# Optimization experiments

Measured on AMD Instinct MI355X. Metric: run time of the kernel, lower is better.

The kernel has to match this reference:

```python
import jax, jax.numpy as jnp
import numpy as np

NUM_REL = 50000
NUM_EDGES = 1000000
DIM_IN = 128
DIM_OUT = 128
NUM_HEAD = 8
DIM_HID = DIM_OUT // NUM_HEAD


def setup_inputs() -> dict:
    key = jax.random.key(0)
    ks = jax.random.split(key, 5)
    emb_rel = jax.random.normal(ks[0], (NUM_REL, DIM_IN), dtype=jnp.float32)
    relation_triplets = jax.random.randint(ks[1], (NUM_EDGES, 3), 0, NUM_REL, dtype=jnp.int64)
    # xavier-normal-ish scales
    attn_w = jax.random.normal(ks[2], (DIM_OUT, 2 * DIM_IN), dtype=jnp.float32) * np.sqrt(2.0 / (DIM_OUT + 2 * DIM_IN))
    attn_b = jnp.zeros((DIM_OUT,), dtype=jnp.float32)
    attn_vec = jax.random.normal(ks[3], (1, NUM_HEAD, DIM_HID), dtype=jnp.float32) * np.sqrt(2.0 / (NUM_HEAD + DIM_HID))
    aggr_w = jax.random.normal(ks[4], (DIM_OUT, DIM_IN), dtype=jnp.float32) * np.sqrt(2.0 / (DIM_OUT + DIM_IN))
    aggr_b = jnp.zeros((DIM_OUT,), dtype=jnp.float32)
    return {"emb_rel": emb_rel, "relation_triplets": relation_triplets,
            "attn_w": attn_w, "attn_b": attn_b, "attn_vec": attn_vec,
            "aggr_w": aggr_w, "aggr_b": aggr_b}


def reference(emb_rel, relation_triplets, attn_w, attn_b, attn_vec, aggr_w, aggr_b):
    num_rel = emb_rel.shape[0]
    head = relation_triplets[:, 0]
    tail = relation_triplets[:, 1]
    h = emb_rel[head]                         # [E, Din]
    t = emb_rel[tail]                         # [E, Din]
    concat = jnp.concatenate([h, t], axis=-1) # [E, 2*Din]
    # per-edge attention logits
    a = jnp.tanh(concat @ attn_w.T + attn_b).reshape(-1, NUM_HEAD, DIM_HID)
    raw = jnp.sum(a * attn_vec, axis=-1)      # [E, H]
    # segment softmax over edges grouped by head relation
    m = jax.ops.segment_max(raw, head, num_segments=num_rel)   # [R, H]
    ev = jnp.exp(raw - m[head])                                # [E, H]
    s = jax.ops.segment_sum(ev, head, num_segments=num_rel)    # [R, H]
    beta = ev / (s[head] + 1e-16)                              # [E, H]
    # weighted aggregation of projected tail embeddings
    msg = (t @ aggr_w.T + aggr_b).reshape(-1, NUM_HEAD, DIM_HID)  # [E, H, Dh]
    out = jax.ops.segment_sum(beta[..., None] * msg, head, num_segments=num_rel)
    return out.reshape(num_rel, NUM_HEAD * DIM_HID)
```

## Files before the change

kernel.cpp:

```cpp
#include <hip/hip_runtime.h>
#include <hip/hip_bf16.h>

#define DIM 128
#define NHEAD 8
#define CAP_B 64
#define NPART 8
#define CAP8 20
#define MAXD 64

typedef __attribute__((ext_vector_type(8))) short short8;
typedef __attribute__((ext_vector_type(4))) float f32x4;
typedef __attribute__((ext_vector_type(4))) int int4v;

__device__ __forceinline__ unsigned short f2bf(float x) {
    unsigned u = __float_as_uint(x);
    unsigned r = (u + 0x7fffu + ((u >> 16) & 1)) >> 16;
    return (unsigned short)r;
}
__device__ __forceinline__ float bf_lo(unsigned v) { return __uint_as_float(v << 16); }
__device__ __forceinline__ float bf_hi(unsigned v) { return __uint_as_float(v & 0xffff0000u); }

__device__ __forceinline__ float fast_tanh(float x) {
    float e = __expf(2.f * x);
    return 1.f - 2.f * __builtin_amdgcn_rcpf(e + 1.f);
}

__global__ __launch_bounds__(256) void partition_kernel(
    const int4v* __restrict__ trip4, unsigned* __restrict__ binbuf,
    int* __restrict__ blockcnt,
    const float* __restrict__ attn_w, const float* __restrict__ aggr_w,
    unsigned short* __restrict__ w16,
    int nE, int nbP1, int BINS)
{
    if ((int)blockIdx.x >= nbP1) {
        int f = (blockIdx.x - nbP1) * 256 + threadIdx.x;
        if (f >= 3 * 128 * 16) return;
        int m   = f / 2048;
        int rem = f - m * 2048;
        int gc  = rem >> 4;
        int k8  = (rem & 15) * 8;
        const float* src = (m == 2) ? &aggr_w[(size_t)gc * 128 + k8]
                                    : &attn_w[(size_t)gc * 256 + m * 128 + k8];
        float4 v0 = *(const float4*)src;
        float4 v1 = *(const float4*)(src + 4);
        short8 r;
        r[0] = (short)f2bf(v0.x); r[1] = (short)f2bf(v0.y);
        r[2] = (short)f2bf(v0.z); r[3] = (short)f2bf(v0.w);
        r[4] = (short)f2bf(v1.x); r[5] = (short)f2bf(v1.y);
        r[6] = (short)f2bf(v1.z); r[7] = (short)f2bf(v1.w);
        *(short8*)&w16[(size_t)f * 8] = r;
        return;
    }

    __shared__ int hist[64];
    __shared__ int base[64];
    __shared__ int tot;
    __shared__ unsigned recs[1024];
    const int tid = threadIdx.x;
    if (tid < 64) hist[tid] = 0;
    __syncthreads();

    int i = blockIdx.x * 256 + tid;
    int e0 = i * 4;
    int h[4] = {-1, -1, -1, -1}, t[4] = {0, 0, 0, 0};
    if (e0 + 3 < nE) {
        int4v v0 = __builtin_nontemporal_load(&trip4[(size_t)i * 3 + 0]);
        int4v v1 = __builtin_nontemporal_load(&trip4[(size_t)i * 3 + 1]);
        int4v v2 = __builtin_nontemporal_load(&trip4[(size_t)i * 3 + 2]);
        h[0] = v0.x; t[0] = v0.y; h[1] = v0.w; t[1] = v1.x;
        h[2] = v1.z; t[2] = v1.w; h[3] = v2.y; t[3] = v2.z;
    } else if (e0 < nE) {
        const int* trip = (const int*)trip4;
#pragma unroll
        for (int j = 0; j < 4; ++j)
            if (e0 + j < nE) { h[j] = trip[(size_t)(e0 + j) * 3]; t[j] = trip[(size_t)(e0 + j) * 3 + 1]; }
    }

    int bn[4], ofs[4];
#pragma unroll
    for (int j = 0; j < 4; ++j) {
        if (h[j] >= 0) {
            bn[j]  = h[j] >> 10;
            ofs[j] = atomicAdd(&hist[bn[j]], 1);
        }
    }
    __syncthreads();

    if (tid < 64) {
        int v = hist[tid];
        int x = v;
#pragma unroll
        for (int d = 1; d < 64; d <<= 1) {
            int y = __shfl_up(x, d);
            if (tid >= d) x += y;
        }
        base[tid] = x - v;
        if (tid == 63) tot = x;
    }
    __syncthreads();

#pragma unroll
    for (int j = 0; j < 4; ++j)
        if (h[j] >= 0) recs[base[bn[j]] + ofs[j]] = ((unsigned)h[j] << 16) | (unsigned)t[j];
    __syncthreads();

    const int total = tot;
    for (int idx = tid; idx < total; idx += 256) {
        unsigned r = recs[idx];
        int b    = (int)(r >> 26);
        int slot = idx - base[b];
        if (slot < CAP_B)
            binbuf[((size_t)b * nbP1 + blockIdx.x) * CAP_B + slot] = r;
    }
    if (tid < BINS) blockcnt[(size_t)tid * nbP1 + blockIdx.x] = min(hist[tid], CAP_B);
}

__global__ __launch_bounds__(256) void binscatter_kernel(
    const unsigned* __restrict__ binbuf, const int* __restrict__ blockcnt,
    unsigned short* __restrict__ bucket8,
    int* __restrict__ count8,
    int nR, int nbP1)
{
    __shared__ int lcnt[1024];
    __shared__ unsigned short stag[1024 * CAP8];
    __shared__ short bcs[1024];
    const int tid  = threadIdx.x;
    const int b    = blockIdx.x >> 3;
    const int part = blockIdx.x & (NPART - 1);
    const int hbase = b << 10;

    for (int j = tid; j < 1024; j += 256) lcnt[j] = 0;
    for (int j = tid; j < nbP1; j += 256) bcs[j] = (short)blockcnt[(size_t)b * nbP1 + j];
    __syncthreads();

    const int nSeg = (nbP1 > part) ? (nbP1 - part + NPART - 1) / NPART : 0;
    const int totSlots = nSeg * CAP_B;
    for (int f = tid; f < totSlots; f += 256) {
        int k = f >> 6;
        int s = f & 63;
        int j = part + NPART * k;
        if (s < (int)bcs[j]) {
            unsigned r = binbuf[((size_t)b * nbP1 + j) * CAP_B + s];
            int rel  = (int)(r >> 16) - hbase;
            int slot = atomicAdd(&lcnt[rel], 1);
            if (slot < CAP8) stag[rel * CAP8 + slot] = (unsigned short)(r & 0xffffu);
        }
    }
    __syncthreads();

    unsigned* dstw = (unsigned*)(bucket8 + ((size_t)part * nR + hbase) * CAP8);
    const unsigned* srcw = (const unsigned*)stag;
    const int nHead = min(1024, nR - hbase);
    const int nW = nHead * (CAP8 / 2);
    for (int j = tid; j < nW; j += 256) dstw[j] = srcw[j];
    for (int rel = tid; rel < nHead; rel += 256)
        count8[(size_t)part * nR + hbase + rel] = min(lcnt[rel], CAP8);
}

__global__ __launch_bounds__(256) void mfma_precompute_kernel(
    const float* __restrict__ emb,
    const unsigned short* __restrict__ w16,
    const float* __restrict__ attn_b,
    const float* __restrict__ aggr_b,
    unsigned short* __restrict__ hW16,
    unsigned short* __restrict__ twm,
    int R)
{
    const int row0 = blockIdx.x * 64;
    const int wave = threadIdx.x >> 6;
    const int lane = threadIdx.x & 63;
    const int lrow = lane & 15;
    const int kg   = lane >> 4;
    const int kbase = kg * 8;

    short8 a[4][4];
#pragma unroll
    for (int rt = 0; rt < 4; ++rt) {
        int r = row0 + rt * 16 + lrow;
        const float* arow = &emb[(size_t)(r < R ? r : R - 1) * 128];
#pragma unroll
        for (int kk = 0; kk < 4; ++kk) {
            float4 v0 = *(const float4*)&arow[kk * 32 + kbase];
            float4 v1 = *(const float4*)&arow[kk * 32 + kbase + 4];
            short8 av;
            av[0] = (short)f2bf(v0.x); av[1] = (short)f2bf(v0.y);
            av[2] = (short)f2bf(v0.z); av[3] = (short)f2bf(v0.w);
            av[4] = (short)f2bf(v1.x); av[5] = (short)f2bf(v1.y);
            av[6] = (short)f2bf(v1.z); av[7] = (short)f2bf(v1.w);
            a[rt][kk] = av;
        }
    }

    for (int m = 0; m < 3; ++m) {
#pragma unroll
        for (int ct2 = 0; ct2 < 2; ++ct2) {
            const int gc = (wave * 2 + ct2) * 16 + lrow;
            const unsigned short* wrow = &w16[((size_t)m * 128 + gc) * 128];
            f32x4 acc[4];
#pragma unroll
            for (int rt = 0; rt < 4; ++rt) acc[rt] = (f32x4){0.f, 0.f, 0.f, 0.f};
#pragma unroll
            for (int kk = 0; kk < 4; ++kk) {
                short8 bfr = *(const short8*)&wrow[kk * 32 + kbase];
#pragma unroll
                for (int rt = 0; rt < 4; ++rt)
                    acc[rt] = __builtin_amdgcn_mfma_f32_16x16x32_bf16(a[rt][kk], bfr, acc[rt], 0, 0, 0);
            }
            float bv = (m == 0) ? attn_b[gc] : ((m == 2) ? aggr_b[gc] : 0.f);
#pragma unroll
            for (int rt = 0; rt < 4; ++rt) {
#pragma unroll
                for (int reg = 0; reg < 4; ++reg) {
                    int gr = row0 + rt * 16 + kg * 4 + reg;
                    if (gr < R) {
                        unsigned short val = f2bf(acc[rt][reg] + bv);
                        if (m == 0) {
                            hW16[(size_t)gr * 128 + gc] = val;
                        } else {
                            twm[(size_t)gr * 256 + (gc >> 1) * 4 + (gc & 1) + ((m == 2) ? 2 : 0)] = val;
                        }
                    }
                }
            }
        }
    }
}

__global__ __launch_bounds__(256) void head_fused_kernel(
    const int* __restrict__ count8,
    const unsigned short* __restrict__ bucket8,
    const unsigned* __restrict__ hW16,
    const unsigned* __restrict__ twm,
    const float* __restrict__ attn_vec,
    const unsigned short* __restrict__ msg16_unused,
    float* __restrict__ out,
    int nR)
{
    const int w    = threadIdx.x >> 6;
    const int h    = blockIdx.x * 4 + w;
    if (h >= nR) return;
    const int lane = threadIdx.x & 63;
    const int d0 = lane * 2;

    const float2 av = *(const float2*)&attn_vec[d0];

    int cv = (lane < NPART) ? min(count8[(size_t)lane * nR + h], CAP8) : 0;
    int c[NPART];
#pragma unroll
    for (int j = 0; j < NPART; ++j) c[j] = __shfl(cv, j);
    int cnt = 0;
#pragma unroll
    for (int j = 0; j < NPART; ++j) cnt += c[j];
    cnt = min(cnt, MAXD);

    float s = 0.f, acc0 = 0.f, acc1 = 0.f;

    if (cnt > 0) {
        unsigned vh = hW16[(size_t)h * 64 + lane];
        const float hx = bf_lo(vh), hy = bf_hi(vh);

        float A = fabsf(av.x) + fabsf(av.y);
        A += __shfl_xor(A, 1);
        A += __shfl_xor(A, 2);
        A += __shfl_xor(A, 4);
        const float m = A;

        int idx = min(lane, cnt - 1);
        int x = 0, p = 0, P = 0;
#pragma unroll
        for (int j = 0; j < NPART - 1; ++j) {
            P += c[j];
            bool go = idx >= P;
            x = go ? j + 1 : x;
            p = go ? P : p;
        }
        int myt = (int)bucket8[((size_t)x * nR + h) * CAP8 + (idx - p)];

        int i = 0;
        for (; i + 4 <= cnt; i += 4) {
            int t0 = __shfl(myt, i),     t1 = __shfl(myt, i + 1);
            int t2 = __shfl(myt, i + 2), t3 = __shfl(myt, i + 3);
            uint2 v0 = *(const uint2*)&twm[(size_t)t0 * 128 + lane * 2];
            uint2 v1 = *(const uint2*)&twm[(size_t)t1 * 128 + lane * 2];
            uint2 v2 = *(const uint2*)&twm[(size_t)t2 * 128 + lane * 2];
            uint2 v3 = *(const uint2*)&twm[(size_t)t3 * 128 + lane * 2];

            float p0 = fast_tanh(hx + bf_lo(v0.x)) * av.x + fast_tanh(hy + bf_hi(v0.x)) * av.y;
            float p1 = fast_tanh(hx + bf_lo(v1.x)) * av.x + fast_tanh(hy + bf_hi(v1.x)) * av.y;
            float p2 = fast_tanh(hx + bf_lo(v2.x)) * av.x + fast_tanh(hy + bf_hi(v2.x)) * av.y;
            float p3 = fast_tanh(hx + bf_lo(v3.x)) * av.x + fast_tanh(hy + bf_hi(v3.x)) * av.y;
            p0 += __shfl_xor(p0, 1); p1 += __shfl_xor(p1, 1);
            p2 += __shfl_xor(p2, 1); p3 += __shfl_xor(p3, 1);
            p0 += __shfl_xor(p0, 2); p1 += __shfl_xor(p1, 2);
            p2 += __shfl_xor(p2, 2); p3 += __shfl_xor(p3, 2);
            p0 += __shfl_xor(p0, 4); p1 += __shfl_xor(p1, 4);
            p2 += __shfl_xor(p2, 4); p3 += __shfl_xor(p3, 4);

            float e0 = __expf(p0 - m), e1 = __expf(p1 - m);
            float e2 = __expf(p2 - m), e3 = __expf(p3 - m);
            s += (e0 + e1) + (e2 + e3);
            acc0 += e0 * bf_lo(v0.y) + e1 * bf_lo(v1.y) + e2 * bf_lo(v2.y) + e3 * bf_lo(v3.y);
            acc1 += e0 * bf_hi(v0.y) + e1 * bf_hi(v1.y) + e2 * bf_hi(v2.y) + e3 * bf_hi(v3.y);
        }
        for (; i < cnt; ++i) {
            int t0 = __shfl(myt, i);
            uint2 v0 = *(const uint2*)&twm[(size_t)t0 * 128 + lane * 2];
            float p0 = fast_tanh(hx + bf_lo(v0.x)) * av.x + fast_tanh(hy + bf_hi(v0.x)) * av.y;
            p0 += __shfl_xor(p0, 1);
            p0 += __shfl_xor(p0, 2);
            p0 += __shfl_xor(p0, 4);
            float e0 = __expf(p0 - m);
            s += e0;
            acc0 += e0 * bf_lo(v0.y);
            acc1 += e0 * bf_hi(v0.y);
        }
    }

    float inv = 1.f / (s + 1e-16f);
    float2 o; o.x = acc0 * inv; o.y = acc1 * inv;
    *(float2*)&out[(size_t)h * 128 + d0] = o;
}

extern "C" void kernel_launch(void* const* d_in, const int* in_sizes, int n_in,
                              void* d_out, int out_size, void* d_ws, size_t ws_size,
                              hipStream_t stream) {
    const float* emb      = (const float*)d_in[0];
    const int*   trip     = (const int*)d_in[1];
    const float* attn_w   = (const float*)d_in[2];
    const float* attn_b   = (const float*)d_in[3];
    const float* attn_vec = (const float*)d_in[4];
    const float* aggr_w   = (const float*)d_in[5];
    const float* aggr_b   = (const float*)d_in[6];
    float*       out      = (float*)d_out;

    const int nR   = in_sizes[0] / DIM;
    const int nE   = in_sizes[1] / 3;
    const int nbP1 = (nE + 1023) / 1024;
    const int BINS = (nR + 1023) >> 10;
    const int nbW  = (3 * 128 * 16 + 255) / 256;

    unsigned short* hW16    = (unsigned short*)d_ws;
    unsigned short* twm     = hW16 + (size_t)nR * 128;
    unsigned short* w16     = twm + (size_t)nR * 256;
    unsigned short* bucket8 = w16 + (size_t)3 * 128 * 128;
    int*            count8  = (int*)(bucket8 + (size_t)NPART * nR * CAP8);
    unsigned*       binbuf  = (unsigned*)(count8 + (size_t)NPART * nR);
    int*            blockcnt= (int*)(binbuf + (size_t)BINS * nbP1 * CAP_B);

    partition_kernel<<<nbP1 + nbW, 256, 0, stream>>>(
        (const int4v*)trip, binbuf, blockcnt, attn_w, aggr_w, w16, nE, nbP1, BINS);
    binscatter_kernel<<<BINS * NPART, 256, 0, stream>>>(binbuf, blockcnt,
                                                        bucket8, count8, nR, nbP1);
    mfma_precompute_kernel<<<(nR + 63) / 64, 256, 0, stream>>>(
        emb, w16, attn_b, aggr_b, hW16, twm, nR);
    head_fused_kernel<<<(nR + 3) / 4, 256, 0, stream>>>(
        count8, bucket8, (const unsigned*)hW16, (const unsigned*)twm,
        attn_vec, (const unsigned short*)nullptr, out, nR);
}
```

Measured before the change: 143.6 us.

## Split wave into two half-waves processing two edges each with 16-byte loads

The per-head aggregation kernel now has each 32-lane half-wave handle a separate edge, with every lane covering 4 feature columns through 16-byte loads instead of 2 columns through 8-byte loads. The head reduction needs one fewer shuffle step, and the two halves are combined by a cross-half shuffle before a single float4 store. Exponentials are rewritten as exp2f with folded log2e constants. This aims to cut per-edge shuffle and instruction overhead and widen memory accesses, at the cost of masked wasted work when the edge count is not a multiple of four.

After: 147.3 us. +2.5%, slower.

```diff
diff --git a/kernel.cpp b/kernel.cpp
--- a/kernel.cpp
+++ b/kernel.cpp
@@ -11,6 +11,9 @@
 typedef __attribute__((ext_vector_type(8))) short short8;
 typedef __attribute__((ext_vector_type(4))) float f32x4;
 typedef __attribute__((ext_vector_type(4))) int int4v;
+typedef __attribute__((ext_vector_type(4))) unsigned uint4v;
+
+#define L2E 1.4426950408889634f
 
 __device__ __forceinline__ unsigned short f2bf(float x) {
     unsigned u = __float_as_uint(x);
@@ -21,7 +24,7 @@
 __device__ __forceinline__ float bf_hi(unsigned v) { return __uint_as_float(v & 0xffff0000u); }
 
 __device__ __forceinline__ float fast_tanh(float x) {
-    float e = __expf(2.f * x);
+    float e = exp2f(x * 2.885390081777927f);
     return 1.f - 2.f * __builtin_amdgcn_rcpf(e + 1.f);
 }
 
@@ -232,7 +235,6 @@
     const unsigned* __restrict__ hW16,
     const unsigned* __restrict__ twm,
     const float* __restrict__ attn_vec,
-    const unsigned short* __restrict__ msg16_unused,
     float* __restrict__ out,
     int nR)
 {
@@ -240,9 +242,8 @@
     const int h    = blockIdx.x * 4 + w;
     if (h >= nR) return;
     const int lane = threadIdx.x & 63;
-    const int d0 = lane * 2;
-
-    const float2 av = *(const float2*)&attn_vec[d0];
+    const int half = lane >> 5;
+    const int l5   = lane & 31;
 
     int cv = (lane < NPART) ? min(count8[(size_t)lane * nR + h], CAP8) : 0;
     int c[NPART];
@@ -253,17 +254,19 @@
     for (int j = 0; j < NPART; ++j) cnt += c[j];
     cnt = min(cnt, MAXD);
 
-    float s = 0.f, acc0 = 0.f, acc1 = 0.f;
+    const float4 av4 = *(const float4*)&attn_vec[l5 * 4];
+    float sacc = 0.f, acc0 = 0.f, acc1 = 0.f, acc2 = 0.f, acc3 = 0.f;
 
     if (cnt > 0) {
-        unsigned vh = hW16[(size_t)h * 64 + lane];
-        const float hx = bf_lo(vh), hy = bf_hi(vh);
-
-        float A = fabsf(av.x) + fabsf(av.y);
+        const uint2* hwrow = (const uint2*)(hW16 + (size_t)h * 64);
+        uint2 hp = hwrow[l5];
+        const float hx0 = bf_lo(hp.x), hx1 = bf_hi(hp.x);
+        const float hx2 = bf_lo(hp.y), hx3 = bf_hi(hp.y);
+
+        float A = fabsf(av4.x) + fabsf(av4.y) + fabsf(av4.z) + fabsf(av4.w);
         A += __shfl_xor(A, 1);
         A += __shfl_xor(A, 2);
-        A += __shfl_xor(A, 4);
-        const float m = A;
+        const float qm = A * L2E;
 
         int idx = min(lane, cnt - 1);
         int x = 0, p = 0, P = 0;
@@ -276,49 +279,50 @@
         }
         int myt = (int)bucket8[((size_t)x * nR + h) * CAP8 + (idx - p)];
 
-        int i = 0;
-        for (; i + 4 <= cnt; i += 4) {
-            int t0 = __shfl(myt, i),     t1 = __shfl(myt, i + 1);
-            int t2 = __shfl(myt, i + 2), t3 = __shfl(myt, i + 3);
-            uint2 v0 = *(const uint2*)&twm[(size_t)t0 * 128 + lane * 2];
-            uint2 v1 = *(const uint2*)&twm[(size_t)t1 * 128 + lane * 2];
-            uint2 v2 = *(const uint2*)&twm[(size_t)t2 * 128 + lane * 2];
-            uint2 v3 = *(const uint2*)&twm[(size_t)t3 * 128 + lane * 2];
-
-            float p0 = fast_tanh(hx + bf_lo(v0.x)) * av.x + fast_tanh(hy + bf_hi(v0.x)) * av.y;
-            float p1 = fast_tanh(hx + bf_lo(v1.x)) * av.x + fast_tanh(hy + bf_hi(v1.x)) * av.y;
-            float p2 = fast_tanh(hx + bf_lo(v2.x)) * av.x + fast_tanh(hy + bf_hi(v2.x)) * av.y;
-            float p3 = fast_tanh(hx + bf_lo(v3.x)) * av.x + fast_tanh(hy + bf_hi(v3.x)) * av.y;
-            p0 += __shfl_xor(p0, 1); p1 += __shfl_xor(p1, 1);
-            p2 += __shfl_xor(p2, 1); p3 += __shfl_xor(p3, 1);
-            p0 += __shfl_xor(p0, 2); p1 += __shfl_xor(p1, 2);
-            p2 += __shfl_xor(p2, 2); p3 += __shfl_xor(p3, 2);
-            p0 += __shfl_xor(p0, 4); p1 += __shfl_xor(p1, 4);
-            p2 += __shfl_xor(p2, 4); p3 += __shfl_xor(p3, 4);
-
-            float e0 = __expf(p0 - m), e1 = __expf(p1 - m);
-            float e2 = __expf(p2 - m), e3 = __expf(p3 - m);
-            s += (e0 + e1) + (e2 + e3);
-            acc0 += e0 * bf_lo(v0.y) + e1 * bf_lo(v1.y) + e2 * bf_lo(v2.y) + e3 * bf_lo(v3.y);
-            acc1 += e0 * bf_hi(v0.y) + e1 * bf_hi(v1.y) + e2 * bf_hi(v2.y) + e3 * bf_hi(v3.y);
-        }
-        for (; i < cnt; ++i) {
-            int t0 = __shfl(myt, i);
-            uint2 v0 = *(const uint2*)&twm[(size_t)t0 * 128 + lane * 2];
-            float p0 = fast_tanh(hx + bf_lo(v0.x)) * av.x + fast_tanh(hy + bf_hi(v0.x)) * av.y;
-            p0 += __shfl_xor(p0, 1);
-            p0 += __shfl_xor(p0, 2);
-            p0 += __shfl_xor(p0, 4);
-            float e0 = __expf(p0 - m);
-            s += e0;
-            acc0 += e0 * bf_lo(v0.y);
-            acc1 += e0 * bf_hi(v0.y);
-        }
-    }
-
-    float inv = 1.f / (s + 1e-16f);
-    float2 o; o.x = acc0 * inv; o.y = acc1 * inv;
-    *(float2*)&out[(size_t)h * 128 + d0] = o;
+        const int npairs = (cnt + 1) >> 1;
+        for (int i2 = 0; i2 < npairs; i2 += 2) {
+            int eA = 2 * i2 + half;
+            int eB = eA + 2;
+            int tA = __shfl(myt, eA);
+            int tB = __shfl(myt, eB);
+            bool vA = eA < cnt, vB = eB < cnt;
+
+            uint4v a4 = *(const uint4v*)(twm + (size_t)tA * 128 + l5 * 4);
+            uint4v b4 = *(const uint4v*)(twm + (size_t)tB * 128 + l5 * 4);
+
+            float pA = fast_tanh(hx0 + bf_lo(a4.x)) * av4.x
+                     + fast_tanh(hx1 + bf_hi(a4.x)) * av4.y
+                     + fast_tanh(hx2 + bf_lo(a4.z)) * av4.z
+                     + fast_tanh(hx3 + bf_hi(a4.z)) * av4.w;
+            float pB = fast_tanh(hx0 + bf_lo(b4.x)) * av4.x
+                     + fast_tanh(hx1 + bf_hi(b4.x)) * av4.y
+                     + fast_tanh(hx2 + bf_lo(b4.z)) * av4.z
+                     + fast_tanh(hx3 + bf_hi(b4.z)) * av4.w;
+            pA += __shfl_xor(pA, 1); pB += __shfl_xor(pB, 1);
+            pA += __shfl_xor(pA, 2); pB += __shfl_xor(pB, 2);
+
+            float eva = vA ? exp2f(fmaf(pA, L2E, -qm)) : 0.f;
+            float evb = vB ? exp2f(fmaf(pB, L2E, -qm)) : 0.f;
+            sacc += eva + evb;
+            acc0 += eva * bf_lo(a4.y) + evb * bf_lo(b4.y);
+            acc1 += eva * bf_hi(a4.y) + evb * bf_hi(b4.y);
+            acc2 += eva * bf_lo(a4.w) + evb * bf_lo(b4.w);
+            acc3 += eva * bf_hi(a4.w) + evb * bf_hi(b4.w);
+        }
+    }
+
+    sacc += __shfl_xor(sacc, 32);
+    acc0 += __shfl_xor(acc0, 32);
+    acc1 += __shfl_xor(acc1, 32);
+    acc2 += __shfl_xor(acc2, 32);
+    acc3 += __shfl_xor(acc3, 32);
+
+    if (half == 0) {
+        float inv = 1.f / (sacc + 1e-16f);
+        float4 o;
+        o.x = acc0 * inv; o.y = acc1 * inv; o.z = acc2 * inv; o.w = acc3 * inv;
+        *(float4*)&out[(size_t)h * 128 + l5 * 4] = o;
+    }
 }
 
 extern "C" void kernel_launch(void* const* d_in, const int* in_sizes, int n_in,
@@ -355,5 +359,5 @@
         emb, w16, attn_b, aggr_b, hW16, twm, nR);
     head_fused_kernel<<<(nR + 3) / 4, 256, 0, stream>>>(
         count8, bucket8, (const unsigned*)hW16, (const unsigned*)twm,
-        attn_vec, (const unsigned short*)nullptr, out, nR);
-}
+        attn_vec, out, nR);
+}
```
